# Kernel optimization log

Hardware: AMD Instinct MI355X
Metric: run time of the kernel (lower is better)

The kernel has to match this reference:

```python
import jax, jax.numpy as jnp
import numpy as np

N = 1_000_000
D = 128
S = 16384


def setup_inputs() -> dict:
    key = jax.random.key(0)
    k_x, k_idx, k_w, k_b = jax.random.split(key, 4)
    x = jax.random.normal(k_x, (N, D), dtype=jnp.float32)
    index = jnp.sort(jax.random.randint(k_idx, (N,), 0, S, dtype=jnp.int64))
    # single plain Linear layer of PyG MLP([D, D], plain_last=True)
    lim = 1.0 / np.sqrt(D)
    W = jax.random.uniform(k_w, (D, D), dtype=jnp.float32, minval=-lim, maxval=lim)
    b = jax.random.uniform(k_b, (D,), dtype=jnp.float32, minval=-lim, maxval=lim)
    return {"x": x, "W": W, "b": b, "index": index, "num_segments": S}


def reference(x, W, b, index, num_segments):
    # att = MLP(x): single plain linear layer (no activation, plain_last=True)
    att = x @ W.T + b  # [N, D]
    # segment softmax over nodes within each graph, per channel (PyG softmax)
    seg_max = jax.ops.segment_max(att, index, num_segments=num_segments)  # [S, D]
    e = jnp.exp(att - seg_max[index])  # [N, D]
    seg_sum = jax.ops.segment_sum(e, index, num_segments=num_segments)  # [S, D]
    att = e / (seg_sum[index] + 1e-16)  # [N, D]
    # attention-weighted global add pool
    return jax.ops.segment_sum(x * att, index, num_segments=num_segments)  # [S, D]
```

## Files before the change

### kernel.cpp

```cpp
#include <hip/hip_runtime.h>
#include <hip/hip_bf16.h>

#define SEGS   16384
#define DCH    128
#define CHUNK  32
#define SEGPB  4
#define FPITCH 132
#define XHBLK  520
#define LOG2E  1.4426950408889634f

using f32x4  = __attribute__((ext_vector_type(4))) float;
using bf16x8 = __attribute__((ext_vector_type(8))) short;
using u32x2  = __attribute__((ext_vector_type(2))) unsigned int;
using u32x4  = __attribute__((ext_vector_type(4))) unsigned int;

__device__ __forceinline__ float u2f(unsigned int u) { return __uint_as_float(u); }
__device__ __forceinline__ unsigned int f2u(float f) { return __float_as_uint(f); }

__global__ void setup_kernel(const float* __restrict__ W,
                             const int* __restrict__ index, int N,
                             unsigned short* __restrict__ WfH,
                             int* __restrict__ seg_start) {
  int i = blockIdx.x * blockDim.x + threadIdx.x;
  if (i < DCH * DCH) {
    int n = i >> 7, k = i & 127;
    float w = W[i] * LOG2E;
    unsigned int u = f2u(w);
    unsigned int r = (u + 0x7FFFu + ((u >> 16) & 1)) >> 16;
    int kt    = k >> 5;
    int ntile = n >> 4;
    int lane  = (n & 15) + 16 * ((k >> 3) & 3);
    int j     = k & 7;
    int dst = ((kt * 8 + ntile) * 64 + lane) * 8 + j;
    WfH[dst] = (unsigned short)r;
  } else if (i < DCH * DCH + SEGS + 1) {
    int s = i - DCH * DCH;
    int lo = 0, hi = N;
    while (lo < hi) {
      int mid = (lo + hi) >> 1;
      if (index[mid] < s) lo = mid + 1; else hi = mid;
    }
    seg_start[s] = lo;
  }
}

__global__ __launch_bounds__(256) void pool_kernel(
    const float* __restrict__ x, const float* __restrict__ bias,
    const int* __restrict__ seg_start,
    const u32x4* __restrict__ WfH,
    float* __restrict__ out) {
  __shared__ unsigned short xh[8 * XHBLK];
  __shared__ float          xf[CHUNK * FPITCH];

  const int t    = threadIdx.x;
  const int wv   = t >> 6;
  const int lane = t & 63;
  const int cl   = lane & 15;
  const int g    = lane >> 4;
  const int k31  = t & 31;
  const int lrow = t >> 5;
  const int lcol = k31 << 2;

  const int xh_base = 1040 * (k31 >> 3) + 8 * lrow + 128 * ((k31 >> 1) & 3) + 4 * (k31 & 1);
  const int xf_base = lrow * FPITCH + lcol;
  const int frag_base = lane * 8;
  const int ex_base   = g * 4 * FPITCH + wv * 32 + cl;

  u32x4 bh[4][2];
#pragma unroll
  for (int kt = 0; kt < 4; ++kt)
#pragma unroll
    for (int nt = 0; nt < 2; ++nt) {
      int off = (kt * 8 + (wv * 2 + nt)) * 64 + lane;
      bh[kt][nt] = WfH[off];
    }

  const float bc0 = bias[wv * 32 + cl]      * LOG2E;
  const float bc1 = bias[wv * 32 + 16 + cl] * LOG2E;

  const int s0   = blockIdx.x * SEGPB;
  const int sEnd = s0 + SEGPB;
  const int R0   = seg_start[s0];
  const int R1   = seg_start[sEnd];

  if (R0 == R1) {
    if (lane < 16) {
      for (int es = s0; es < sEnd; ++es) {
        out[(size_t)es * DCH + wv * 32 + cl]      = 0.f;
        out[(size_t)es * DCH + wv * 32 + 16 + cl] = 0.f;
      }
    }
    return;
  }

  int curSeg = s0;
  int segEnd = seg_start[curSeg + 1];
  int c0 = R0;

  f32x4 pvA[4], pvB[4];
  auto issue = [&](f32x4 (&pv)[4], int base) {
#pragma unroll
    for (int p = 0; p < 4; ++p) {
      int lr = base + lrow + p * 8;
      f32x4 v = {0.f, 0.f, 0.f, 0.f};
      if (lr < R1) v = *(const f32x4*)(x + (size_t)lr * DCH + lcol);
      pv[p] = v;
    }
  };

  issue(pvA, R0);
  if (R0 + CHUNK < R1) issue(pvB, R0 + CHUNK);

  float den[2] = {0.f, 0.f};
  float num[2] = {0.f, 0.f};

  auto body = [&](f32x4 (&pvS)[4]) -> bool {
#pragma unroll
    for (int p = 0; p < 4; ++p) {
      f32x4 v = pvS[p];
      unsigned int u0 = f2u(v[0]), u1 = f2u(v[1]), u2 = f2u(v[2]), u3 = f2u(v[3]);
      u32x2 H = { (u1 & 0xFFFF0000u) | (u0 >> 16),
                  (u3 & 0xFFFF0000u) | (u2 >> 16) };
      *(u32x2*)&xh[xh_base + (p >> 1) * XHBLK + (p & 1) * 64] = H;
      *(f32x4*)&xf[xf_base + p * 8 * FPITCH] = v;
    }

    if (c0 + 2 * CHUNK < R1) issue(pvS, c0 + 2 * CHUNK);

    asm volatile("s_waitcnt lgkmcnt(0)" ::: "memory");
    __builtin_amdgcn_sched_barrier(0);
    __builtin_amdgcn_s_barrier();
    __builtin_amdgcn_sched_barrier(0);

    f32x4 Cf[2][2];
#pragma unroll
    for (int mt = 0; mt < 2; ++mt) {
      Cf[mt][0] = (f32x4){bc0, bc0, bc0, bc0};
      Cf[mt][1] = (f32x4){bc1, bc1, bc1, bc1};
    }
#pragma unroll
    for (int kt = 0; kt < 4; ++kt) {
      u32x4 ah[2];
#pragma unroll
      for (int mt = 0; mt < 2; ++mt)
        ah[mt] = *(const u32x4*)&xh[frag_base + (2 * kt + mt) * XHBLK];
#pragma unroll
      for (int mt = 0; mt < 2; ++mt)
#pragma unroll
        for (int nt = 0; nt < 2; ++nt) {
          bf16x8 A = __builtin_bit_cast(bf16x8, ah[mt]);
          bf16x8 B = __builtin_bit_cast(bf16x8, bh[kt][nt]);
          Cf[mt][nt] = __builtin_amdgcn_mfma_f32_16x16x32_bf16(A, B, Cf[mt][nt], 0, 0, 0);
        }
    }

    float pr[2][2][4], xv[2][2][4];
#pragma unroll
    for (int nt = 0; nt < 2; ++nt)
#pragma unroll
      for (int mt = 0; mt < 2; ++mt)
#pragma unroll
        for (int r = 0; r < 4; ++r) {
          pr[nt][mt][r] = __builtin_amdgcn_exp2f(Cf[mt][nt][r]);
          xv[nt][mt][r] = xf[ex_base + (mt * 16 + r) * FPITCH + nt * 16];
        }

    const int lim = c0 + CHUNK;
    int lo = c0;
    while (curSeg < sEnd) {
      const int hi  = segEnd;
      const int hiC = (hi < lim) ? hi : lim;
#pragma unroll
      for (int nt = 0; nt < 2; ++nt)
#pragma unroll
        for (int mt = 0; mt < 2; ++mt)
#pragma unroll
          for (int r = 0; r < 4; ++r) {
            const int row = c0 + mt * 16 + g * 4 + r;
            const bool use = (row >= lo) & (row < hiC);
            const float pp = use ? pr[nt][mt][r] : 0.f;
            den[nt] += pp;
            num[nt] += pp * xv[nt][mt][r];
          }
      if (hi <= lim) {
#pragma unroll
        for (int nt = 0; nt < 2; ++nt) {
          float l = den[nt], a = num[nt];
          l += __shfl_xor(l, 16); l += __shfl_xor(l, 32);
          a += __shfl_xor(a, 16); a += __shfl_xor(a, 32);
          if (lane < 16)
            out[(size_t)curSeg * DCH + wv * 32 + nt * 16 + cl] = a / (l + 1e-16f);
          den[nt] = 0.f; num[nt] = 0.f;
        }
        lo = hi;
        ++curSeg;
        if (curSeg < sEnd) segEnd = seg_start[curSeg + 1];
      } else {
        break;
      }
    }
    if (curSeg >= sEnd) return false;
    c0 += CHUNK;

    asm volatile("s_waitcnt lgkmcnt(0)" ::: "memory");
    __builtin_amdgcn_sched_barrier(0);
    __builtin_amdgcn_s_barrier();
    __builtin_amdgcn_sched_barrier(0);
    return true;
  };

  for (;;) {
    if (!body(pvA)) break;
    if (!body(pvB)) break;
  }
}

extern "C" void kernel_launch(void* const* d_in, const int* in_sizes, int n_in,
                              void* d_out, int out_size, void* d_ws, size_t ws_size,
                              hipStream_t stream) {
  const float* x    = (const float*)d_in[0];
  const float* W    = (const float*)d_in[1];
  const float* bias = (const float*)d_in[2];
  const int*   idx  = (const int*)d_in[3];
  const int N = in_sizes[0] / DCH;

  unsigned short* WfH = (unsigned short*)d_ws;
  int* seg = (int*)(WfH + DCH * DCH);

  int setup_threads = DCH * DCH + SEGS + 1;
  setup_kernel<<<(setup_threads + 255) / 256, 256, 0, stream>>>(W, idx, N, WfH, seg);
  pool_kernel<<<SEGS / SEGPB, 256, 0, stream>>>(x, bias, seg,
                                                (const u32x4*)WfH,
                                                (float*)d_out);
}
```

Before: 133.7 us.

## Double-buffer bf16 LDS tile, drop fp32 LDS copy, gather x from global

The fp32 shared-memory copy of x is removed. The values needed for the weighted sum are now loaded straight from global memory (expected to hit L2/L1) in the MFMA output layout. The bf16 tile is double-buffered in LDS, which removes the second barrier per chunk, and prefetch depth drops from two chunks to one. This cuts LDS traffic and synchronisation, but adds scalar strided global loads and shortens the distance over which prefetches can hide latency.

```diff
diff --git a/kernel.cpp b/kernel.cpp
--- a/kernel.cpp
+++ b/kernel.cpp
@@ -3,9 +3,9 @@
 
 #define SEGS   16384
 #define DCH    128
+#define NROWS  1000000
 #define CHUNK  32
 #define SEGPB  4
-#define FPITCH 132
 #define XHBLK  520
 #define LOG2E  1.4426950408889634f
 
@@ -49,8 +49,7 @@
     const int* __restrict__ seg_start,
     const u32x4* __restrict__ WfH,
     float* __restrict__ out) {
-  __shared__ unsigned short xh[8 * XHBLK];
-  __shared__ float          xf[CHUNK * FPITCH];
+  __shared__ unsigned short xh[2][8 * XHBLK];
 
   const int t    = threadIdx.x;
   const int wv   = t >> 6;
@@ -62,9 +61,8 @@
   const int lcol = k31 << 2;
 
   const int xh_base = 1040 * (k31 >> 3) + 8 * lrow + 128 * ((k31 >> 1) & 3) + 4 * (k31 & 1);
-  const int xf_base = lrow * FPITCH + lcol;
   const int frag_base = lane * 8;
-  const int ex_base   = g * 4 * FPITCH + wv * 32 + cl;
+  const int ch0 = wv * 32 + cl;
 
   u32x4 bh[4][2];
 #pragma unroll
@@ -75,8 +73,8 @@
       bh[kt][nt] = WfH[off];
     }
 
-  const float bc0 = bias[wv * 32 + cl]      * LOG2E;
-  const float bc1 = bias[wv * 32 + 16 + cl] * LOG2E;
+  const float bc0 = bias[ch0]      * LOG2E;
+  const float bc1 = bias[ch0 + 16] * LOG2E;
 
   const int s0   = blockIdx.x * SEGPB;
   const int sEnd = s0 + SEGPB;
@@ -97,8 +95,8 @@
   int segEnd = seg_start[curSeg + 1];
   int c0 = R0;
 
-  f32x4 pvA[4], pvB[4];
-  auto issue = [&](f32x4 (&pv)[4], int base) {
+  f32x4 pv[4];
+  auto issue = [&](int base) {
 #pragma unroll
     for (int p = 0; p < 4; ++p) {
       int lr = base + lrow + p * 8;
@@ -108,24 +106,34 @@
     }
   };
 
-  issue(pvA, R0);
-  if (R0 + CHUNK < R1) issue(pvB, R0 + CHUNK);
+  issue(R0);
 
   float den[2] = {0.f, 0.f};
   float num[2] = {0.f, 0.f};
 
-  auto body = [&](f32x4 (&pvS)[4]) -> bool {
+  auto body = [&](unsigned short* XH) -> bool {
 #pragma unroll
     for (int p = 0; p < 4; ++p) {
-      f32x4 v = pvS[p];
+      f32x4 v = pv[p];
       unsigned int u0 = f2u(v[0]), u1 = f2u(v[1]), u2 = f2u(v[2]), u3 = f2u(v[3]);
       u32x2 H = { (u1 & 0xFFFF0000u) | (u0 >> 16),
                   (u3 & 0xFFFF0000u) | (u2 >> 16) };
-      *(u32x2*)&xh[xh_base + (p >> 1) * XHBLK + (p & 1) * 64] = H;
-      *(f32x4*)&xf[xf_base + p * 8 * FPITCH] = v;
-    }
-
-    if (c0 + 2 * CHUNK < R1) issue(pvS, c0 + 2 * CHUNK);
+      *(u32x2*)&XH[xh_base + (p >> 1) * XHBLK + (p & 1) * 64] = H;
+    }
+
+    float gx[2][2][4];
+#pragma unroll
+    for (int mt = 0; mt < 2; ++mt)
+#pragma unroll
+      for (int r = 0; r < 4; ++r) {
+        int row = c0 + mt * 16 + g * 4 + r;
+        row = (row < NROWS) ? row : (NROWS - 1);
+        const float* rp = x + (size_t)row * DCH;
+        gx[0][mt][r] = rp[ch0];
+        gx[1][mt][r] = rp[ch0 + 16];
+      }
+
+    if (c0 + CHUNK < R1) issue(c0 + CHUNK);
 
     asm volatile("s_waitcnt lgkmcnt(0)" ::: "memory");
     __builtin_amdgcn_sched_barrier(0);
@@ -143,7 +151,7 @@
       u32x4 ah[2];
 #pragma unroll
       for (int mt = 0; mt < 2; ++mt)
-        ah[mt] = *(const u32x4*)&xh[frag_base + (2 * kt + mt) * XHBLK];
+        ah[mt] = *(const u32x4*)&XH[frag_base + (2 * kt + mt) * XHBLK];
 #pragma unroll
       for (int mt = 0; mt < 2; ++mt)
 #pragma unroll
@@ -154,16 +162,14 @@
         }
     }
 
-    float pr[2][2][4], xv[2][2][4];
+    float pr[2][2][4];
 #pragma unroll
     for (int nt = 0; nt < 2; ++nt)
 #pragma unroll
       for (int mt = 0; mt < 2; ++mt)
 #pragma unroll
-        for (int r = 0; r < 4; ++r) {
+        for (int r = 0; r < 4; ++r)
           pr[nt][mt][r] = __builtin_amdgcn_exp2f(Cf[mt][nt][r]);
-          xv[nt][mt][r] = xf[ex_base + (mt * 16 + r) * FPITCH + nt * 16];
-        }
 
     const int lim = c0 + CHUNK;
     int lo = c0;
@@ -180,7 +186,7 @@
             const bool use = (row >= lo) & (row < hiC);
             const float pp = use ? pr[nt][mt][r] : 0.f;
             den[nt] += pp;
-            num[nt] += pp * xv[nt][mt][r];
+            num[nt] += pp * gx[nt][mt][r];
           }
       if (hi <= lim) {
 #pragma unroll
@@ -201,17 +207,12 @@
     }
     if (curSeg >= sEnd) return false;
     c0 += CHUNK;
-
-    asm volatile("s_waitcnt lgkmcnt(0)" ::: "memory");
-    __builtin_amdgcn_sched_barrier(0);
-    __builtin_amdgcn_s_barrier();
-    __builtin_amdgcn_sched_barrier(0);
     return true;
   };
 
   for (;;) {
-    if (!body(pvA)) break;
-    if (!body(pvB)) break;
+    if (!body(&xh[0][0])) break;
+    if (!body(&xh[1][0])) break;
   }
 }
 
```

Measured after the change: 130.9 us. 2.1% less time.
